# Kernel tuning notes

Hardware: AMD Instinct MI355X
Metric: run time of the kernel (lower is better)

The kernel has to match this reference:

```python
import jax, jax.numpy as jnp
import numpy as np

D = 4096
L = 24
H = 8
HD = D // H
Z_TAU = 3.0
SCALE = 1.0 / float(np.sqrt(HD))


def _ln(x, w=None, b=None, eps=1e-5):
    # torch F.layer_norm over last dim; affine optional
    m = jnp.mean(x, axis=-1, keepdims=True)
    v = jnp.var(x, axis=-1, keepdims=True)
    y = (x - m) * jax.lax.rsqrt(v + eps)
    if w is not None:
        y = y * w + b
    return y


def setup_inputs() -> dict:
    key = jax.random.key(0)
    ks = jax.random.split(key, 16)
    T, N = 512, 2048
    s = 0.02  # init scale for weights
    inp = {
        'text_features': jax.random.normal(ks[0], (T, D), jnp.float32),
        'layer_features': jax.random.normal(ks[1], (L, N, D), jnp.float32),
        # DynamicSharingUnit params
        'layer_embed': jax.random.normal(ks[2], (L, D), jnp.float32) * s,
        'Wc_w': jax.random.normal(ks[3], (2 * D, D), jnp.float32) * s,
        'Wc_b': jnp.zeros((D,), jnp.float32),
        'Wz_w': jax.random.normal(ks[4], (4 * D, D), jnp.float32) * s,
        'Wz_b': jnp.full((D,), -2.0, jnp.float32),
        # SpatialGate params (delta MLP + alpha)
        'd1_w': jax.random.normal(ks[5], (D, D), jnp.float32) * s,
        'd1_b': jnp.zeros((D,), jnp.float32),
        'd2_w': jax.random.normal(ks[6], (D, D), jnp.float32) * s,
        'd2_b': jnp.zeros((D,), jnp.float32),
        'alpha': jnp.asarray(0.5, jnp.float32),
        # attention projections
        'Wq_w': jax.random.normal(ks[7], (D, D), jnp.float32) * s,
        'Wq_b': jnp.zeros((D,), jnp.float32),
        'Wk_w': jax.random.normal(ks[8], (D, D), jnp.float32) * s,
        'Wk_b': jnp.zeros((D,), jnp.float32),
        'Wo_w': jax.random.normal(ks[9], (D, D), jnp.float32) * s,
        'Wo_b': jnp.zeros((D,), jnp.float32),
        # layernorm affine params
        'qn_w': jnp.ones((D,), jnp.float32), 'qn_b': jnp.zeros((D,), jnp.float32),
        'kn_w': jnp.ones((D,), jnp.float32), 'kn_b': jnp.zeros((D,), jnp.float32),
        'vn_w': jnp.ones((D,), jnp.float32), 'vn_b': jnp.zeros((D,), jnp.float32),
        'on_w': jnp.ones((D,), jnp.float32), 'on_b': jnp.zeros((D,), jnp.float32),
    }
    return inp


def reference(text_features, layer_features, layer_embed, Wc_w, Wc_b, Wz_w, Wz_b,
              d1_w, d1_b, d2_w, d2_b, alpha,
              Wq_w, Wq_b, Wk_w, Wk_b, Wo_w, Wo_b,
              qn_w, qn_b, kn_w, kn_b, vn_w, vn_b, on_w, on_b):
    T = text_features.shape[0]
    dt = text_features.dtype

    text_global = _ln(jnp.mean(text_features, axis=0))  # [D]
    y = jnp.mean(layer_features, axis=1)                # [L, D] per-layer means

    # sequential 24-step DynamicSharingUnit recurrence
    def step(c_prev, xs):
        y_l, e_l = xs
        c_tilde = jnp.tanh(jnp.concatenate([y_l, e_l], axis=-1) @ Wc_w + Wc_b)
        z_logit = jnp.concatenate([y_l, c_prev, e_l, text_global], axis=-1) @ Wz_w + Wz_b
        z = jax.nn.sigmoid(z_logit / Z_TAU)
        c_l = c_prev + z * (c_tilde - c_prev)
        return c_l, c_l

    c0 = jnp.zeros((D,), dt)
    _, contexts = jax.lax.scan(step, c0, (y, layer_embed))  # [L, D]

    c_23 = contexts[-2]            # context after layer index 22
    pre_23 = layer_features[-2]    # [N, D]

    # SpatialGate: x + tanh(alpha) * tanh(MLP(LN(x + c)))
    h = _ln(pre_23 + c_23[None, :])
    delta = jnp.tanh(jax.nn.gelu(h @ d1_w + d1_b, approximate=False) @ d2_w + d2_b)
    refreshed = pre_23 + jnp.tanh(alpha) * delta  # [N, D]

    Q = _ln(text_features @ Wq_w + Wq_b, qn_w, qn_b)  # [T, D]
    K = _ln(refreshed @ Wk_w + Wk_b, kn_w, kn_b)      # [N, D]
    V = _ln(refreshed, vn_w, vn_b)                    # [N, D]

    q = Q.reshape(T, H, HD)
    k = K.reshape(-1, H, HD)
    v = V.reshape(-1, H, HD)
    scores = jnp.einsum('thd,nhd->htn', q, k) * SCALE  # [H, T, N]
    w = jax.nn.softmax(scores, axis=-1)
    attn = jnp.einsum('htn,nhd->thd', w, v).reshape(T, D)

    return _ln(attn @ Wo_w + Wo_b, on_w, on_b)  # [T, D]
```

## Files before the change

kernel.cpp:

```cpp
#include <hip/hip_runtime.h>
#include <hip/hip_bf16.h>

constexpr int D_  = 4096;
constexpr int L_  = 24;
constexpr int T_  = 512;
constexpr int N_  = 2048;
constexpr int H_  = 8;
constexpr int HD_ = 512;
constexpr float SCALE_ = 0.04419417382415922f;

typedef __attribute__((ext_vector_type(8))) short short8;
typedef __attribute__((ext_vector_type(4))) float f32x4;

__device__ __forceinline__ unsigned short f2b(float f){
  union{float f; unsigned u;} v; v.f=f;
  return (unsigned short)((v.u + 0x7fffu + ((v.u>>16)&1u))>>16);
}
__device__ __forceinline__ float b2f(unsigned short h){
  union{unsigned u; float f;} v; v.u=((unsigned)h)<<16; return v.f;
}

__device__ __forceinline__ void gload_lds16(const unsigned short* g, unsigned short* l){
  __builtin_amdgcn_global_load_lds((const __attribute__((address_space(1))) unsigned int*)g,
                                   (__attribute__((address_space(3))) unsigned int*)l, 16, 0, 0);
}

struct TP5 { const float* in[5]; unsigned short* out[5]; };

__global__ void prepass_all(TP5 a, const float* __restrict__ wzc_f,
                            unsigned short* __restrict__ wzcb,
                            const float* __restrict__ text,
                            unsigned short* __restrict__ txb){
  const int z = blockIdx.z, t = threadIdx.x;
  if(z < 5){
    __shared__ float tile[64][65];
    const float* in = a.in[z];
    unsigned short* out = a.out[z];
    const int k0 = blockIdx.x*64, n0 = blockIdx.y*64;
    const int rr = t>>4, cc = (t&15)*4;
#pragma unroll
    for(int i=0;i<4;++i){
      const int row = i*16 + rr;
      const float4 v = *(const float4*)(in + (size_t)(k0+row)*D_ + n0 + cc);
      tile[row][cc]=v.x; tile[row][cc+1]=v.y; tile[row][cc+2]=v.z; tile[row][cc+3]=v.w;
    }
    __syncthreads();
#pragma unroll
    for(int i=0;i<4;++i){
      const int row = i*16 + rr;
      unsigned short o4[4] __attribute__((aligned(8)));
      o4[0]=f2b(tile[cc  ][row]);
      o4[1]=f2b(tile[cc+1][row]);
      o4[2]=f2b(tile[cc+2][row]);
      o4[3]=f2b(tile[cc+3][row]);
      *(unsigned long long*)&out[(size_t)(n0+row)*D_ + k0 + cc] = *(const unsigned long long*)o4;
    }
  } else {
    const int bb = blockIdx.y*64 + blockIdx.x;
    const float* in; unsigned short* out; size_t base;
    if(z < 7){ in = wzc_f; out = wzcb; base = ((size_t)(z-5)*4096 + bb)*2048 + (size_t)t*8; }
    else { if(bb >= 1024) return; in = text; out = txb; base = (size_t)bb*2048 + (size_t)t*8; }
    const float4 x0 = *(const float4*)(in + base);
    const float4 x1 = *(const float4*)(in + base + 4);
    unsigned short o[8] __attribute__((aligned(16)));
    o[0]=f2b(x0.x);o[1]=f2b(x0.y);o[2]=f2b(x0.z);o[3]=f2b(x0.w);
    o[4]=f2b(x1.x);o[5]=f2b(x1.y);o[6]=f2b(x1.z);o[7]=f2b(x1.w);
    *(uint4*)(out + base) = *(const uint4*)o;
  }
}

__global__ void transpose_head_b(const unsigned short* __restrict__ in,
                                 unsigned short* __restrict__ out){
  __shared__ unsigned short tile[64][65];
  const int t = threadIdx.x;
  const int h = blockIdx.z;
  const int d0 = blockIdx.x*64, n0 = blockIdx.y*64;
  const int tr = t>>6, tc = t&63;
#pragma unroll
  for(int i=0;i<16;++i) tile[i*4+tr][tc] = in[(size_t)(n0+i*4+tr)*D_ + h*HD_ + d0+tc];
  __syncthreads();
#pragma unroll
  for(int i=0;i<16;++i) out[((size_t)h*HD_ + d0+i*4+tr)*N_ + n0+tc] = tile[tc][i*4+tr];
}

__global__ void colsum_all(const float* __restrict__ layers, const float* __restrict__ text,
                           float* __restrict__ part){
  const int d4 = (blockIdx.x*256 + threadIdx.x)*4;
  const int s = blockIdx.y, z = blockIdx.z;
  const float* p; int rows;
  if(z < 23){ p = layers + (size_t)z*N_*D_ + (size_t)s*(N_/8)*D_ + d4; rows = N_/8; }
  else      { p = text + (size_t)s*(T_/8)*D_ + d4; rows = T_/8; }
  float4 a = {0.f,0.f,0.f,0.f};
  for(int r=0;r<rows;++r){
    const float4 v = *(const float4*)(p + (size_t)r*D_);
    a.x += v.x; a.y += v.y; a.z += v.z; a.w += v.w;
  }
  *(float4*)&part[((size_t)z*8 + s)*D_ + d4] = a;
}

__global__ void reduce_y_gm(const float* __restrict__ part, float* __restrict__ y,
                            float* __restrict__ tg){
  __shared__ float sm[256];
  const int b = blockIdx.x, t = threadIdx.x;
  if(b < 368){
    const int i = b*256 + t, l = i>>12, j = i & (D_-1);
    float a = 0.f;
#pragma unroll
    for(int s=0;s<8;++s) a += part[((size_t)l*8 + s)*D_ + j];
    y[i] = a * (1.f/N_);
    return;
  }
  float v[16]; float sum = 0.f;
#pragma unroll
  for(int c=0;c<16;++c){
    const int j = c*256 + t;
    float a = 0.f;
#pragma unroll
    for(int s=0;s<8;++s) a += part[((size_t)184 + s)*D_ + j];
    v[c] = a * (1.f/T_); sum += v[c];
  }
  sm[t]=sum; __syncthreads();
  for(int o=128;o>0;o>>=1){ if(t<o) sm[t]+=sm[t+o]; __syncthreads(); }
  const float mean = sm[0]*(1.f/D_); __syncthreads();
  float q=0.f;
#pragma unroll
  for(int c=0;c<16;++c){ const float dd=v[c]-mean; q+=dd*dd; }
  sm[t]=q; __syncthreads();
  for(int o=128;o>0;o>>=1){ if(t<o) sm[t]+=sm[t+o]; __syncthreads(); }
  const float rstd = rsqrtf(sm[0]*(1.f/D_) + 1e-5f);
#pragma unroll
  for(int c=0;c<16;++c) tg[c*256+t] = (v[c]-mean)*rstd;
}

__global__ void smallm_all(const float* __restrict__ Wc, const float* __restrict__ Wz,
                           const float* __restrict__ y, const float* __restrict__ e,
                           const float* __restrict__ tg,
                           float* __restrict__ part0, float* __restrict__ part1){
  const int j = (blockIdx.x*256 + threadIdx.x)*2;
  const int sIdx = blockIdx.y;
  const bool w1 = (sIdx >= 16);
  const int s = w1 ? sIdx-16 : sIdx;
  const float* W = w1 ? Wz : Wc;
  const int k0 = s * 512;
  float a0[L_], a1[L_];
#pragma unroll
  for(int l=0;l<L_;++l){ a0[l]=0.f; a1[l]=0.f; }
  __shared__ float xs[L_][64];
  for(int kc=0; kc<512; kc+=64){
    __syncthreads();
    for(int i=threadIdx.x; i<L_*64; i+=256){
      const int l=i>>6, kk=i&63, k=k0+kc+kk;
      float xv;
      if(!w1) xv = (k<D_)? y[(size_t)l*D_+k] : e[(size_t)l*D_ + (k-D_)];
      else    xv = (k<D_)? y[(size_t)l*D_+k]
                : ((k<2*D_)? e[(size_t)l*D_ + (k-D_)] : tg[k-2*D_]);
      xs[l][kk]=xv;
    }
    __syncthreads();
    for(int kk=0;kk<64;++kk){
      const int k=k0+kc+kk;
      const int wrow = w1 ? ((k<D_)? k : k+D_) : k;
      const float2 wv = *(const float2*)&W[(size_t)wrow*D_ + j];
#pragma unroll
      for(int l=0;l<L_;++l){ a0[l] += xs[l][kk]*wv.x; a1[l] += xs[l][kk]*wv.y; }
    }
  }
  float* out = w1 ? part1 : part0;
  const int S = w1 ? 24 : 16;
  for(int l=0;l<L_;++l){
    float2 o; o.x=a0[l]; o.y=a1[l];
    *(float2*)&out[((size_t)l*S + s)*D_ + j] = o;
  }
}

__global__ void reduce_ct_aall(const float* __restrict__ part0, const float* __restrict__ part1,
                               const float* __restrict__ Wcb, const float* __restrict__ Wzb,
                               float* __restrict__ ct, float* __restrict__ aall){
  int b = blockIdx.x;
  const int t = threadIdx.x;
  if(b < 368){
    const int i = b*256+t, l = i>>12, j = i & (D_-1);
    float a = 0.f;
#pragma unroll
    for(int s=0;s<16;++s) a += part0[((size_t)l*16 + s)*D_ + j];
    ct[i] = tanhf(a + Wcb[j]);
  } else {
    b -= 368;
    const int i = b*256+t, l = i>>12, j = i & (D_-1);
    float a = 0.f;
#pragma unroll
    for(int s=0;s<24;++s) a += part1[((size_t)l*24 + s)*D_ + j];
    aall[i] = a + Wzb[j];
  }
}

__device__ __forceinline__ void rec_matvec(const unsigned short* __restrict__ Wzc,
                                           const float* cs, float* red, float* __restrict__ zcur,
                                           int cg, int ks, int t){
  const int k0 = ks*128;
  float acc[8];
#pragma unroll
  for(int q=0;q<8;++q) acc[q]=0.f;
  const int rg = t>>6, oc = t&63;
  const unsigned short* Wb = Wzc + (size_t)(k0+rg*32)*D_ + cg*512 + oc*8;
#pragma unroll
  for(int rr=0;rr<4;++rr){
#pragma unroll
    for(int r=0;r<8;++r){
      const uint4 wv = *(const uint4*)(Wb + (size_t)(rr*8+r)*D_);
      const float cv = cs[rg*32+rr*8+r];
      acc[0]+=cv*b2f((unsigned short)(wv.x&0xffffu));
      acc[1]+=cv*b2f((unsigned short)(wv.x>>16));
      acc[2]+=cv*b2f((unsigned short)(wv.y&0xffffu));
      acc[3]+=cv*b2f((unsigned short)(wv.y>>16));
      acc[4]+=cv*b2f((unsigned short)(wv.z&0xffffu));
      acc[5]+=cv*b2f((unsigned short)(wv.z>>16));
      acc[6]+=cv*b2f((unsigned short)(wv.w&0xffffu));
      acc[7]+=cv*b2f((unsigned short)(wv.w>>16));
    }
  }
#pragma unroll
  for(int q=0;q<8;++q) red[rg*512 + oc*8 + q] = acc[q];
  __syncthreads();
  float s0=0.f, s1=0.f;
#pragma unroll
  for(int g=0;g<4;++g){ s0 += red[g*512 + t]; s1 += red[g*512 + t + 256]; }
  zcur[(size_t)ks*D_ + cg*512 + t]       = s0;
  zcur[(size_t)ks*D_ + cg*512 + t + 256] = s1;
}

__global__ __launch_bounds__(256,2) void rec_first(
    const unsigned short* __restrict__ Wzc, const float* __restrict__ aall0,
    const float* __restrict__ ct0, float* __restrict__ zcur, float* __restrict__ cnew){
  const int blk = blockIdx.x, cg = blk & 7, ks = blk >> 3, t = threadIdx.x;
  const int k0 = ks*128;
  __shared__ float cs[128];
  __shared__ float red[4*512];
  if(t<128){
    const float zl = aall0[k0+t];
    const float z = 1.f/(1.f+expf(-zl*(1.f/3.f)));
    const float cn = z*ct0[k0+t];
    cs[t]=cn; if(cg==0) cnew[k0+t]=cn;
  }
  __syncthreads();
  rec_matvec(Wzc, cs, red, zcur, cg, ks, t);
}

__global__ __launch_bounds__(256,2) void rec_step(
    const unsigned short* __restrict__ Wzc,
    const float* __restrict__ zprev, float* __restrict__ zcur,
    const float* __restrict__ cprev, float* __restrict__ cnew,
    const float* __restrict__ aallL, const float* __restrict__ ctL){
  const int blk = blockIdx.x, cg = blk & 7, ks = blk >> 3, t = threadIdx.x;
  const int k0 = ks*128;
  __shared__ float cs[128];
  __shared__ float red[4*512];
  {
    const int col = t & 127, hf = t >> 7;
    float s=0.f;
#pragma unroll
    for(int si=0;si<16;++si) s += zprev[(size_t)(hf*16+si)*D_ + k0 + col];
    red[hf*128+col] = s;
    __syncthreads();
    if(t<128){
      const float zl = aallL[k0+t] + red[t] + red[128+t];
      const float z = 1.f/(1.f+expf(-zl*(1.f/3.f)));
      const float cp = cprev[k0+t];
      const float cn = cp + z*(ctL[k0+t]-cp);
      cs[t]=cn;
      if(cg==0) cnew[k0+t]=cn;
    }
  }
  __syncthreads();
  rec_matvec(Wzc, cs, red, zcur, cg, ks, t);
}

__global__ void gate_final(const float* __restrict__ zp, const float* __restrict__ cin,
                           const float* __restrict__ aallL, const float* __restrict__ ctL,
                           float* __restrict__ cout){
  const int j = blockIdx.x*256 + threadIdx.x;
  float zl = aallL[j];
  for(int s=0;s<32;++s) zl += zp[(size_t)s*D_ + j];
  const float z = 1.f/(1.f + expf(-zl*(1.f/3.f)));
  const float cp = cin[j];
  cout[j] = cp + z*(ctL[j] - cp);
}

__device__ __forceinline__ void ln_vals(float* v, const float* w, const float* b,
                                        float* of, unsigned short* ob,
                                        bool aff, bool obf, float* sm, int t){
  float s=0.f;
#pragma unroll
  for(int i=0;i<16;++i) s += v[i];
  sm[t]=s; __syncthreads();
  for(int o=128;o>0;o>>=1){ if(t<o) sm[t]+=sm[t+o]; __syncthreads(); }
  const float mean = sm[0]*(1.f/D_); __syncthreads();
  float q=0.f;
#pragma unroll
  for(int i=0;i<16;++i){ const float dd=v[i]-mean; q+=dd*dd; }
  sm[t]=q; __syncthreads();
  for(int o=128;o>0;o>>=1){ if(t<o) sm[t]+=sm[t+o]; __syncthreads(); }
  const float rstd = rsqrtf(sm[0]*(1.f/D_) + 1e-5f);
#pragma unroll
  for(int i=0;i<16;++i){
    const int d = i*256+t;
    float yv=(v[i]-mean)*rstd;
    if(aff) yv = yv*w[d] + b[d];
    if(obf) ob[d] = f2b(yv);
    else    of[d] = yv;
  }
}

template<bool ADDC, bool AFF, bool OBF>
__global__ void row_ln(const float* __restrict__ x, const float* __restrict__ cvec,
                       const float* __restrict__ w, const float* __restrict__ b,
                       float* __restrict__ of, unsigned short* __restrict__ ob){
  __shared__ float sm[256];
  const int row = blockIdx.x, t = threadIdx.x;
  const float* xr = x + (size_t)row*D_;
  float v[16];
#pragma unroll
  for(int i=0;i<16;++i){
    const int d = i*256 + t;
    float val = xr[d];
    if(ADDC) val += cvec[d];
    v[i]=val;
  }
  ln_vals(v, w, b, of? of + (size_t)row*D_ : nullptr,
          ob? ob + (size_t)row*D_ : nullptr, AFF, OBF, sm, t);
}

__global__ void ln3(const float* __restrict__ qpre, const float* __restrict__ refr,
                    const float* __restrict__ kpre, const float* __restrict__ qpb,
                    const float* __restrict__ qnw, const float* __restrict__ qnb,
                    const float* __restrict__ vnw, const float* __restrict__ vnb,
                    const float* __restrict__ knw, const float* __restrict__ knb,
                    unsigned short* __restrict__ qb, unsigned short* __restrict__ vb,
                    unsigned short* __restrict__ kb){
  __shared__ float sm[256];
  const int which = blockIdx.y, row = blockIdx.x, t = threadIdx.x;
  float v[16];
  if(which==0){
    if(row>=T_) return;
    const float* x0 = qpre + (size_t)row*D_;
#pragma unroll
    for(int i=0;i<16;++i){
      const int d = i*256+t;
      v[i] = x0[d] + x0[(size_t)T_*D_ + d] + x0[(size_t)2*T_*D_ + d]
           + x0[(size_t)3*T_*D_ + d] + qpb[d];
    }
    ln_vals(v, qnw, qnb, nullptr, qb + (size_t)row*D_, true, true, sm, t);
  } else {
    const float* x = (which==1)? refr : kpre;
    const float* w = (which==1)? vnw : knw;
    const float* b = (which==1)? vnb : knb;
    unsigned short* o = (which==1)? vb : kb;
    const float* xr = x + (size_t)row*D_;
#pragma unroll
    for(int i=0;i<16;++i) v[i] = xr[i*256+t];
    ln_vals(v, w, b, nullptr, o + (size_t)row*D_, true, true, sm, t);
  }
}

__global__ void row_ln_out(const float* __restrict__ opre, const float* __restrict__ opb,
                           const float* __restrict__ w, const float* __restrict__ b,
                           float* __restrict__ out){
  __shared__ float sm[256];
  const int row = blockIdx.x, t = threadIdx.x;
  const float* x0 = opre + (size_t)row*D_;
  float v[16];
#pragma unroll
  for(int i=0;i<16;++i){
    const int d = i*256+t;
    v[i] = x0[d] + x0[(size_t)T_*D_ + d] + x0[(size_t)2*T_*D_ + d]
         + x0[(size_t)3*T_*D_ + d] + opb[d];
  }
  ln_vals(v, w, b, out + (size_t)row*D_, nullptr, true, false, sm, t);
}

__global__ void softmax_rows(unsigned short* __restrict__ wb){
  __shared__ float sm[256];
  const size_t base = (size_t)blockIdx.x * N_;
  const int t = threadIdx.x;
  float v[8];
  float mx = -3.4e38f;
#pragma unroll
  for(int i=0;i<8;++i){ v[i]=b2f(wb[base + i*256 + t]); mx=fmaxf(mx,v[i]); }
  sm[t]=mx; __syncthreads();
  for(int o=128;o>0;o>>=1){ if(t<o) sm[t]=fmaxf(sm[t],sm[t+o]); __syncthreads(); }
  mx=sm[0]; __syncthreads();
  float s=0.f;
#pragma unroll
  for(int i=0;i<8;++i){ v[i]=expf(v[i]-mx); s+=v[i]; }
  sm[t]=s; __syncthreads();
  for(int o=128;o>0;o>>=1){ if(t<o) sm[t]+=sm[t+o]; __syncthreads(); }
  const float inv = 1.f/sm[0];
#pragma unroll
  for(int i=0;i<8;++i) wb[base + i*256 + t] = f2b(v[i]*inv);
}

enum { EPI_F32_BIAS=0, EPI_BF16_GELU=1, EPI_SPATIAL=2, EPI_BF16_SCALE=3, EPI_BF16=4, EPI_F32_RAW=5 };

constexpr int GBK=32;

template<int EPI, int WM>
__global__ __launch_bounds__(256,2) void gemm_bt(
  const unsigned short* __restrict__ A, const unsigned short* __restrict__ BT,
  const float* __restrict__ bias,
  float* __restrict__ Cf, unsigned short* __restrict__ Cb,
  int M, int Ncols, int K, int lda, int ldb, int ldc,
  long long aZ, long long bZ, long long cZ,
  const float* __restrict__ pre, const float* __restrict__ alphap, float scale)
{
  constexpr int BMt = WM*64;
  constexpr int NF  = WM*2;
  __shared__ unsigned short As[BMt*GBK];
  __shared__ unsigned short Bs[128*GBK];
  const int t = threadIdx.x;
  const int lane = t&63, wid = t>>6;
  const int m0 = blockIdx.x*BMt, n0 = blockIdx.y*128;
  A  += (size_t)blockIdx.z*aZ;
  BT += (size_t)blockIdx.z*bZ;
  const size_t coff = (size_t)blockIdx.z*cZ;

  const int srow = wid*16 + (lane>>2);
  const int scol = (lane&3)*8;
  const unsigned short* ag = A  + (size_t)(m0+srow)*lda + scol;
  const unsigned short* bg = BT + (size_t)(n0+srow)*ldb + scol;
  unsigned short* asl = &As[wid*512];
  unsigned short* bsl = &Bs[wid*512];

  f32x4 acc[4][NF];
#pragma unroll
  for(int i=0;i<4;++i)
#pragma unroll
    for(int j=0;j<NF;++j) acc[i][j]=(f32x4){0.f,0.f,0.f,0.f};

  const int wm = (WM==2)? (wid>>1)*64 : 0;
  const int wn = (WM==2)? (wid&1)*64 : wid*32;
  const int lrow=lane&15, lk=(lane>>4)*8;

  for(int k0=0;k0<K;k0+=GBK){
    __syncthreads();
    gload_lds16(ag + k0, asl);
    if(WM==2) gload_lds16(ag + k0 + (size_t)64*lda, asl + 2048);
    gload_lds16(bg + k0, bsl);
    gload_lds16(bg + k0 + (size_t)64*ldb, bsl + 2048);
    __syncthreads();
    short8 af[4], bfr[NF];
#pragma unroll
    for(int i=0;i<4;++i)  af[i]  = *(const short8*)&As[(wm+i*16+lrow)*GBK + lk];
#pragma unroll
    for(int j=0;j<NF;++j) bfr[j] = *(const short8*)&Bs[(wn+j*16+lrow)*GBK + lk];
#pragma unroll
    for(int i=0;i<4;++i)
#pragma unroll
      for(int j=0;j<NF;++j)
        acc[i][j] = __builtin_amdgcn_mfma_f32_16x16x32_bf16(af[i], bfr[j], acc[i][j], 0,0,0);
  }

#pragma unroll
  for(int i=0;i<4;++i)
#pragma unroll
    for(int j=0;j<NF;++j){
      const int col = n0 + wn + j*16 + lrow;
      const int rb  = m0 + wm + i*16 + (lane>>4)*4;
#pragma unroll
      for(int r=0;r<4;++r){
        const int row = rb + r;
        const float v = acc[i][j][r];
        const size_t idx = coff + (size_t)row*ldc + col;
        if(EPI==EPI_F32_BIAS){ Cf[idx] = v + bias[col]; }
        else { Cb[idx]=f2b(v); }
      }
    }
}

constexpr int P_SLOT_A = 128*64;
constexpr int P_SLOT_B = 256*64;
constexpr int P_SLOT_E = P_SLOT_A + P_SLOT_B;

#define MF16(a,b,c) __builtin_amdgcn_mfma_f32_16x16x32_bf16(a,b,c,0,0,0)

template<int EPI, bool SWZ>
__global__ __launch_bounds__(512,2) void gemm8p(
    const unsigned short* __restrict__ A, const unsigned short* __restrict__ BT,
    const float* __restrict__ bias,
    float* __restrict__ Cf, unsigned short* __restrict__ Cb,
    int K, int lda, int ldb, int ldc,
    long long aZ, long long bZ, long long cZ,
    const float* __restrict__ pre, const float* __restrict__ alphap, float scale)
{
  __shared__ unsigned short lds[3*P_SLOT_E];
  const int tid = threadIdx.x;
  const int lane = tid & 63, wid = tid >> 6;
  int mi, ni, zi;
  if(SWZ){
    const int b = blockIdx.x;
    const int swz = (b & 7)*32 + (b >> 3);
    mi = swz >> 4; ni = swz & 15; zi = 0;
  } else { mi = blockIdx.x; ni = blockIdx.y; zi = blockIdx.z; }
  const int m0 = mi*128, n0 = ni*256;
  A  += (size_t)zi*aZ;
  BT += (size_t)zi*bZ;
  const size_t coff = (size_t)zi*cZ;

  const int wm = (wid >> 2)*64, wn = (wid & 3)*64;
  const int lr = lane & 15, lhi = lane >> 4;

  auto stage = [&](int slot, int kt){
    const int k0 = kt*64;
    unsigned short* sA = lds + slot*P_SLOT_E;
    unsigned short* sB = sA + P_SLOT_A;
#pragma unroll
    for(int q=0;q<2;++q){
      const int o = q*8192 + tid*16;
      const int r = o >> 7;
      const int cb = (o & 127) ^ ((r & 7) << 4);
      gload_lds16(A + (size_t)(m0+r)*lda + k0 + (cb>>1), sA + q*4096 + wid*512);
    }
#pragma unroll
    for(int q=0;q<4;++q){
      const int o = q*8192 + tid*16;
      const int r = o >> 7;
      const int cb = (o & 127) ^ ((r & 7) << 4);
      gload_lds16(BT + (size_t)(n0+r)*ldb + k0 + (cb>>1), sB + q*4096 + wid*512);
    }
  };

  auto ldA = [&](const unsigned short* sA, int i, int ks)->short8{
    const int ra = wm + i*16 + lr;
    const int cb = (ks*64 + lhi*16) ^ ((ra & 7) << 4);
    return *(const short8*)((const char*)sA + ra*128 + cb);
  };
  auto ldB = [&](const unsigned short* sB, int j, int ks)->short8{
    const int rb = wn + j*16 + lr;
    const int cb = (ks*64 + lhi*16) ^ ((rb & 7) << 4);
    return *(const short8*)((const char*)sB + rb*128 + cb);
  };

  f32x4 acc[4][4];
#pragma unroll
  for(int i=0;i<4;++i)
#pragma unroll
    for(int j=0;j<4;++j) acc[i][j]=(f32x4){0.f,0.f,0.f,0.f};

  auto tile_compute = [&](const unsigned short* sA, const unsigned short* sB){
#pragma unroll
    for(int ks=0; ks<2; ++ks){
      short8 a0=ldA(sA,0,ks), a1=ldA(sA,1,ks), a2=ldA(sA,2,ks), a3=ldA(sA,3,ks);
      short8 b0=ldB(sB,0,ks), b1=ldB(sB,1,ks);
      __builtin_amdgcn_s_setprio(1);
      acc[0][0]=MF16(a0,b0,acc[0][0]); acc[1][0]=MF16(a1,b0,acc[1][0]);
      acc[2][0]=MF16(a2,b0,acc[2][0]); acc[3][0]=MF16(a3,b0,acc[3][0]);
      acc[0][1]=MF16(a0,b1,acc[0][1]); acc[1][1]=MF16(a1,b1,acc[1][1]);
      acc[2][1]=MF16(a2,b1,acc[2][1]); acc[3][1]=MF16(a3,b1,acc[3][1]);
      __builtin_amdgcn_s_setprio(0);
      __builtin_amdgcn_s_barrier();
      short8 b2=ldB(sB,2,ks), b3=ldB(sB,3,ks);
      __builtin_amdgcn_s_setprio(1);
      acc[0][2]=MF16(a0,b2,acc[0][2]); acc[1][2]=MF16(a1,b2,acc[1][2]);
      acc[2][2]=MF16(a2,b2,acc[2][2]); acc[3][2]=MF16(a3,b2,acc[3][2]);
      acc[0][3]=MF16(a0,b3,acc[0][3]); acc[1][3]=MF16(a1,b3,acc[1][3]);
      acc[2][3]=MF16(a2,b3,acc[2][3]); acc[3][3]=MF16(a3,b3,acc[3][3]);
      __builtin_amdgcn_s_setprio(0);
      if(ks==0) __builtin_amdgcn_s_barrier();
    }
  };

  const int nt = K >> 6;
  stage(0, 0);
  stage(1, 1);
  int cur = 0;
  for(int t=0; t<nt-1; ++t){
    asm volatile("s_waitcnt vmcnt(6)" ::: "memory");
    __builtin_amdgcn_s_barrier();
    int s2 = cur+2; if(s2>=3) s2-=3;
    if(t+2 < nt) stage(s2, t+2);
    const unsigned short* sA = lds + cur*P_SLOT_E;
    tile_compute(sA, sA + P_SLOT_A);
    ++cur; if(cur==3) cur=0;
  }
  asm volatile("s_waitcnt vmcnt(0)" ::: "memory");
  __builtin_amdgcn_s_barrier();
  {
    const unsigned short* sA = lds + cur*P_SLOT_E;
    tile_compute(sA, sA + P_SLOT_A);
  }

  float ta=0.f;
  if(EPI==EPI_SPATIAL) ta = tanhf(alphap[0]);
#pragma unroll
  for(int i=0;i<4;++i)
#pragma unroll
    for(int j=0;j<4;++j){
      const int col = n0 + wn + j*16 + lr;
      const int rb  = m0 + wm + i*16 + lhi*4;
#pragma unroll
      for(int r=0;r<4;++r){
        const int row = rb + r;
        const float v = acc[i][j][r];
        const size_t idx = coff + (size_t)row*ldc + col;
        if(EPI==EPI_F32_BIAS){ Cf[idx] = v + bias[col]; }
        else if(EPI==EPI_F32_RAW){ Cf[idx] = v; }
        else if(EPI==EPI_BF16_GELU){
          const float x = v + bias[col];
          Cb[idx] = f2b(0.5f*x*(1.f+erff(x*0.70710678118f)));
        }
        else if(EPI==EPI_SPATIAL){
          const float x = tanhf(v + bias[col]);
          const float o = pre[idx] + ta*x;
          Cf[idx]=o; Cb[idx]=f2b(o);
        }
        else if(EPI==EPI_BF16_SCALE){ Cb[idx]=f2b(v*scale); }
      }
    }
}

constexpr size_t OFF_TG   = 0;
constexpr size_t OFF_C    = OFF_TG + (size_t)D_*4;
constexpr size_t OFF_Y    = OFF_C  + (size_t)D_*4;
constexpr size_t OFF_CT   = OFF_Y  + (size_t)L_*D_*4;
constexpr size_t OFF_AA   = OFF_CT + (size_t)L_*D_*4;
constexpr size_t OFF_ZP0  = OFF_AA + (size_t)L_*D_*4;
constexpr size_t OFF_ZP1  = OFF_ZP0 + (size_t)32*D_*4;
constexpr size_t OFF_PART = OFF_ZP1 + (size_t)32*D_*4;
constexpr size_t OFF_QPRE = OFF_PART + (size_t)24*L_*D_*4;
constexpr size_t OFF_REFR = OFF_QPRE + (size_t)4*T_*D_*4;
constexpr size_t OFF_HB   = OFF_REFR + (size_t)N_*D_*4;
constexpr size_t OFF_G1   = OFF_HB + (size_t)N_*D_*2;
constexpr size_t OFF_KPRE = OFF_HB;
constexpr size_t OFF_QB   = OFF_G1 + (size_t)N_*D_*2;
constexpr size_t OFF_KB   = OFF_QB + (size_t)T_*D_*2;
constexpr size_t OFF_VB   = OFF_KB + (size_t)N_*D_*2;
constexpr size_t OFF_VT   = OFF_VB + (size_t)N_*D_*2;
constexpr size_t OFF_WB   = OFF_VT + (size_t)H_*HD_*N_*2;
constexpr size_t OFF_ATTN = OFF_WB + (size_t)H_*T_*N_*2;
constexpr size_t OFF_W1T  = OFF_ATTN + (size_t)T_*D_*2;
constexpr size_t OFF_W2T  = OFF_W1T + (size_t)D_*D_*2;
constexpr size_t OFF_WKT  = OFF_W2T + (size_t)D_*D_*2;
constexpr size_t OFF_WQT  = OFF_WKT + (size_t)D_*D_*2;
constexpr size_t OFF_WOT  = OFF_WQT + (size_t)D_*D_*2;
constexpr size_t OFF_WZCB = OFF_WOT + (size_t)D_*D_*2;
constexpr size_t OFF_TXB  = OFF_WZCB + (size_t)D_*D_*2;
constexpr size_t OFF_REFB = OFF_TXB + (size_t)T_*D_*2;
constexpr size_t OFF_CA   = OFF_REFB + (size_t)N_*D_*2;
constexpr size_t OFF_CB   = OFF_CA + (size_t)D_*4;

extern "C" void kernel_launch(void* const* d_in, const int* in_sizes, int n_in,
                              void* d_out, int out_size, void* d_ws, size_t ws_size,
                              hipStream_t stream){
  (void)in_sizes; (void)n_in; (void)out_size; (void)ws_size;
  const float* text  = (const float*)d_in[0];
  const float* layers= (const float*)d_in[1];
  const float* le    = (const float*)d_in[2];
  const float* Wc    = (const float*)d_in[3];
  const float* Wcb   = (const float*)d_in[4];
  const float* Wz    = (const float*)d_in[5];
  const float* Wzb   = (const float*)d_in[6];
  const float* d1w   = (const float*)d_in[7];
  const float* d1b   = (const float*)d_in[8];
  const float* d2w   = (const float*)d_in[9];
  const float* d2b   = (const float*)d_in[10];
  const float* alpha = (const float*)d_in[11];
  const float* Wqw=(const float*)d_in[12]; const float* Wqb=(const float*)d_in[13];
  const float* Wkw=(const float*)d_in[14]; const float* Wkb=(const float*)d_in[15];
  const float* Wow=(const float*)d_in[16]; const float* Wob=(const float*)d_in[17];
  const float* qnw=(const float*)d_in[18]; const float* qnb=(const float*)d_in[19];
  const float* knw=(const float*)d_in[20]; const float* knb=(const float*)d_in[21];
  const float* vnw=(const float*)d_in[22]; const float* vnb=(const float*)d_in[23];
  const float* onw=(const float*)d_in[24]; const float* onb=(const float*)d_in[25];
  float* out = (float*)d_out;

  char* w = (char*)d_ws;
  float* tg    = (float*)(w + OFF_TG);
  float* cvec  = (float*)(w + OFF_C);
  float* y     = (float*)(w + OFF_Y);
  float* ct    = (float*)(w + OFF_CT);
  float* aall  = (float*)(w + OFF_AA);
  float* zp0   = (float*)(w + OFF_ZP0);
  float* zp1   = (float*)(w + OFF_ZP1);
  float* part  = (float*)(w + OFF_PART);
  float* part1 = part + (size_t)384*D_;
  float* qpre  = (float*)(w + OFF_QPRE);
  float* opre  = qpre;
  float* refr  = (float*)(w + OFF_REFR);
  float* kpre  = (float*)(w + OFF_KPRE);
  float* cA    = (float*)(w + OFF_CA);
  float* cB    = (float*)(w + OFF_CB);
  unsigned short* hb    = (unsigned short*)(w + OFF_HB);
  unsigned short* g1    = (unsigned short*)(w + OFF_G1);
  unsigned short* qb    = (unsigned short*)(w + OFF_QB);
  unsigned short* kb    = (unsigned short*)(w + OFF_KB);
  unsigned short* vb    = (unsigned short*)(w + OFF_VB);
  unsigned short* vt    = (unsigned short*)(w + OFF_VT);
  unsigned short* wb    = (unsigned short*)(w + OFF_WB);
  unsigned short* attnb = (unsigned short*)(w + OFF_ATTN);
  unsigned short* d1t   = (unsigned short*)(w + OFF_W1T);
  unsigned short* d2t   = (unsigned short*)(w + OFF_W2T);
  unsigned short* wkt   = (unsigned short*)(w + OFF_WKT);
  unsigned short* wqt   = (unsigned short*)(w + OFF_WQT);
  unsigned short* wot   = (unsigned short*)(w + OFF_WOT);
  unsigned short* wzcb  = (unsigned short*)(w + OFF_WZCB);
  unsigned short* txb   = (unsigned short*)(w + OFF_TXB);
  unsigned short* refb  = (unsigned short*)(w + OFF_REFB);

  const dim3 b256(256);
  const float* pre23 = layers + (size_t)(L_-2)*N_*D_;

  TP5 tp; tp.in[0]=d1w; tp.in[1]=d2w; tp.in[2]=Wkw; tp.in[3]=Wqw; tp.in[4]=Wow;
  tp.out[0]=d1t; tp.out[1]=d2t; tp.out[2]=wkt; tp.out[3]=wqt; tp.out[4]=wot;
  prepass_all<<<dim3(64,64,8),b256,0,stream>>>(tp, Wz + (size_t)D_*D_, wzcb, text, txb);

  colsum_all<<<dim3(4,8,24),b256,0,stream>>>(layers, text, part);
  reduce_y_gm<<<dim3(369),b256,0,stream>>>(part, y, tg);
  smallm_all<<<dim3(8,40),b256,0,stream>>>(Wc, Wz, y, le, tg, part, part1);
  reduce_ct_aall<<<dim3(736),b256,0,stream>>>(part, part1, Wcb, Wzb, ct, aall);

  rec_first<<<dim3(256),b256,0,stream>>>(wzcb, aall, ct, zp0, cA);
  for(int i=1;i<L_-2;++i){
    float* zprev = (i&1)? zp0 : zp1;
    float* zcur  = (i&1)? zp1 : zp0;
    float* cprev = (i&1)? cA  : cB;
    float* cnew  = (i&1)? cB  : cA;
    rec_step<<<dim3(256),b256,0,stream>>>(wzcb, zprev, zcur, cprev, cnew,
        aall + (size_t)i*D_, ct + (size_t)i*D_);
  }
  gate_final<<<dim3(16),b256,0,stream>>>(zp1, cB,
      aall + (size_t)(L_-2)*D_, ct + (size_t)(L_-2)*D_, cvec);

  row_ln<true,false,true><<<dim3(N_),b256,0,stream>>>(pre23, cvec, nullptr,nullptr, nullptr, hb);
  gemm8p<EPI_BF16_GELU,true><<<dim3(256),dim3(512),0,stream>>>(
      hb, d1t, d1b, nullptr, g1, D_, D_, D_, D_, 0,0,0, nullptr,nullptr,0.f);
  gemm8p<EPI_SPATIAL,true><<<dim3(256),dim3(512),0,stream>>>(
      g1, d2t, d2b, refr, refb, D_, D_, D_, D_, 0,0,0, pre23, alpha, 0.f);

  gemm8p<EPI_F32_RAW,false><<<dim3(4,16,4),dim3(512),0,stream>>>(
      txb, wqt, nullptr, qpre, nullptr, 1024, D_, D_, D_,
      1024, 1024, (long long)T_*D_, nullptr,nullptr,0.f);
  gemm8p<EPI_F32_BIAS,true><<<dim3(256),dim3(512),0,stream>>>(
      refb, wkt, Wkb, kpre, nullptr, D_, D_, D_, D_, 0,0,0, nullptr,nullptr,0.f);

  ln3<<<dim3(N_,3),b256,0,stream>>>(qpre, refr, kpre, Wqb,
      qnw,qnb, vnw,vnb, knw,knb, qb, vb, kb);
  transpose_head_b<<<dim3(8,32,8),b256,0,stream>>>(vb, vt);

  gemm8p<EPI_BF16_SCALE,false><<<dim3(4,8,8),dim3(512),0,stream>>>(
      qb, kb, nullptr, nullptr, wb, HD_, D_, D_, N_,
      (long long)HD_, (long long)HD_, (long long)T_*N_, nullptr,nullptr, SCALE_);
  softmax_rows<<<dim3(H_*T_),b256,0,stream>>>(wb);
  gemm_bt<EPI_BF16,1><<<dim3(8,4,8),b256,0,stream>>>(
      wb, vt, nullptr, nullptr, attnb, T_, HD_, N_, N_, N_, D_,
      (long long)T_*N_, (long long)HD_*N_, (long long)HD_, nullptr,nullptr,0.f);

  gemm8p<EPI_F32_RAW,false><<<dim3(4,16,4),dim3(512),0,stream>>>(
      attnb, wot, nullptr, opre, nullptr, 1024, D_, D_, D_,
      1024, 1024, (long long)T_*D_, nullptr,nullptr,0.f);
  row_ln_out<<<dim3(T_),b256,0,stream>>>(opre, Wob, onw, onb, out);
}
```

Baseline: 1.096 ms.

## Overlap weight transpose-conversion with serial recurrence kernels

```diff
diff --git a/kernel.cpp b/kernel.cpp
--- a/kernel.cpp
+++ b/kernel.cpp
@@ -25,47 +25,48 @@
                                    (__attribute__((address_space(3))) unsigned int*)l, 16, 0, 0);
 }
 
+__global__ void cvt_small(const float* __restrict__ wzc_f, unsigned short* __restrict__ wzcb,
+                          const float* __restrict__ text, unsigned short* __restrict__ txb){
+  const int z = blockIdx.z, t = threadIdx.x;
+  const int bb = blockIdx.y*64 + blockIdx.x;
+  const float* in; unsigned short* out; size_t base;
+  if(z < 2){ in = wzc_f; out = wzcb; base = ((size_t)z*4096 + bb)*2048 + (size_t)t*8; }
+  else { if(bb >= 1024) return; in = text; out = txb; base = (size_t)bb*2048 + (size_t)t*8; }
+  const float4 x0 = *(const float4*)(in + base);
+  const float4 x1 = *(const float4*)(in + base + 4);
+  unsigned short o[8] __attribute__((aligned(16)));
+  o[0]=f2b(x0.x);o[1]=f2b(x0.y);o[2]=f2b(x0.z);o[3]=f2b(x0.w);
+  o[4]=f2b(x1.x);o[5]=f2b(x1.y);o[6]=f2b(x1.z);o[7]=f2b(x1.w);
+  *(uint4*)(out + base) = *(const uint4*)o;
+}
+
 struct TP5 { const float* in[5]; unsigned short* out[5]; };
-
-__global__ void prepass_all(TP5 a, const float* __restrict__ wzc_f,
-                            unsigned short* __restrict__ wzcb,
-                            const float* __restrict__ text,
-                            unsigned short* __restrict__ txb){
-  const int z = blockIdx.z, t = threadIdx.x;
-  if(z < 5){
-    __shared__ float tile[64][65];
-    const float* in = a.in[z];
-    unsigned short* out = a.out[z];
-    const int k0 = blockIdx.x*64, n0 = blockIdx.y*64;
-    const int rr = t>>4, cc = (t&15)*4;
-#pragma unroll
-    for(int i=0;i<4;++i){
-      const int row = i*16 + rr;
-      const float4 v = *(const float4*)(in + (size_t)(k0+row)*D_ + n0 + cc);
-      tile[row][cc]=v.x; tile[row][cc+1]=v.y; tile[row][cc+2]=v.z; tile[row][cc+3]=v.w;
-    }
-    __syncthreads();
-#pragma unroll
-    for(int i=0;i<4;++i){
-      const int row = i*16 + rr;
-      unsigned short o4[4] __attribute__((aligned(8)));
-      o4[0]=f2b(tile[cc  ][row]);
-      o4[1]=f2b(tile[cc+1][row]);
-      o4[2]=f2b(tile[cc+2][row]);
-      o4[3]=f2b(tile[cc+3][row]);
-      *(unsigned long long*)&out[(size_t)(n0+row)*D_ + k0 + cc] = *(const unsigned long long*)o4;
-    }
-  } else {
-    const int bb = blockIdx.y*64 + blockIdx.x;
-    const float* in; unsigned short* out; size_t base;
-    if(z < 7){ in = wzc_f; out = wzcb; base = ((size_t)(z-5)*4096 + bb)*2048 + (size_t)t*8; }
-    else { if(bb >= 1024) return; in = text; out = txb; base = (size_t)bb*2048 + (size_t)t*8; }
-    const float4 x0 = *(const float4*)(in + base);
-    const float4 x1 = *(const float4*)(in + base + 4);
-    unsigned short o[8] __attribute__((aligned(16)));
-    o[0]=f2b(x0.x);o[1]=f2b(x0.y);o[2]=f2b(x0.z);o[3]=f2b(x0.w);
-    o[4]=f2b(x1.x);o[5]=f2b(x1.y);o[6]=f2b(x1.z);o[7]=f2b(x1.w);
-    *(uint4*)(out + base) = *(const uint4*)o;
+constexpr int TP_TILES = 5*4096;
+constexpr int TP_CHUNK = 931;
+
+__device__ __forceinline__ void do_transpose_tile(const TP5& a, int idx, float* shm, int t){
+  const int z = idx >> 12, rem = idx & 4095;
+  const int k0 = (rem >> 6)*64, n0 = (rem & 63)*64;
+  const float* in = a.in[z];
+  unsigned short* out = a.out[z];
+  float (*tile)[65] = (float(*)[65])shm;
+  const int rr = t>>4, cc = (t&15)*4;
+#pragma unroll
+  for(int i=0;i<4;++i){
+    const int row = i*16 + rr;
+    const float4 v = *(const float4*)(in + (size_t)(k0+row)*D_ + n0 + cc);
+    tile[row][cc]=v.x; tile[row][cc+1]=v.y; tile[row][cc+2]=v.z; tile[row][cc+3]=v.w;
+  }
+  __syncthreads();
+#pragma unroll
+  for(int i=0;i<4;++i){
+    const int row = i*16 + rr;
+    unsigned short o4[4] __attribute__((aligned(8)));
+    o4[0]=f2b(tile[cc  ][row]);
+    o4[1]=f2b(tile[cc+1][row]);
+    o4[2]=f2b(tile[cc+2][row]);
+    o4[3]=f2b(tile[cc+3][row]);
+    *(unsigned long long*)&out[(size_t)(n0+row)*D_ + k0 + cc] = *(const unsigned long long*)o4;
   }
 }
 
@@ -231,11 +232,18 @@
 
 __global__ __launch_bounds__(256,2) void rec_first(
     const unsigned short* __restrict__ Wzc, const float* __restrict__ aall0,
-    const float* __restrict__ ct0, float* __restrict__ zcur, float* __restrict__ cnew){
-  const int blk = blockIdx.x, cg = blk & 7, ks = blk >> 3, t = threadIdx.x;
+    const float* __restrict__ ct0, float* __restrict__ zcur, float* __restrict__ cnew,
+    TP5 tp, int tbase){
+  __shared__ float shm[64*65];
+  const int blk = blockIdx.x, t = threadIdx.x;
+  if(blk >= 256){
+    const int idx = tbase + blk - 256;
+    if(idx < TP_TILES) do_transpose_tile(tp, idx, shm, t);
+    return;
+  }
+  const int cg = blk & 7, ks = blk >> 3;
   const int k0 = ks*128;
-  __shared__ float cs[128];
-  __shared__ float red[4*512];
+  float* cs = shm; float* red = shm + 128;
   if(t<128){
     const float zl = aall0[k0+t];
     const float z = 1.f/(1.f+expf(-zl*(1.f/3.f)));
@@ -250,11 +258,18 @@
     const unsigned short* __restrict__ Wzc,
     const float* __restrict__ zprev, float* __restrict__ zcur,
     const float* __restrict__ cprev, float* __restrict__ cnew,
-    const float* __restrict__ aallL, const float* __restrict__ ctL){
-  const int blk = blockIdx.x, cg = blk & 7, ks = blk >> 3, t = threadIdx.x;
+    const float* __restrict__ aallL, const float* __restrict__ ctL,
+    TP5 tp, int tbase){
+  __shared__ float shm[64*65];
+  const int blk = blockIdx.x, t = threadIdx.x;
+  if(blk >= 256){
+    const int idx = tbase + blk - 256;
+    if(idx < TP_TILES) do_transpose_tile(tp, idx, shm, t);
+    return;
+  }
+  const int cg = blk & 7, ks = blk >> 3;
   const int k0 = ks*128;
-  __shared__ float cs[128];
-  __shared__ float red[4*512];
+  float* cs = shm; float* red = shm + 128;
   {
     const int col = t & 127, hf = t >> 7;
     float s=0.f;
@@ -710,21 +725,22 @@
 
   TP5 tp; tp.in[0]=d1w; tp.in[1]=d2w; tp.in[2]=Wkw; tp.in[3]=Wqw; tp.in[4]=Wow;
   tp.out[0]=d1t; tp.out[1]=d2t; tp.out[2]=wkt; tp.out[3]=wqt; tp.out[4]=wot;
-  prepass_all<<<dim3(64,64,8),b256,0,stream>>>(tp, Wz + (size_t)D_*D_, wzcb, text, txb);
+
+  cvt_small<<<dim3(64,64,3),b256,0,stream>>>(Wz + (size_t)D_*D_, wzcb, text, txb);
 
   colsum_all<<<dim3(4,8,24),b256,0,stream>>>(layers, text, part);
   reduce_y_gm<<<dim3(369),b256,0,stream>>>(part, y, tg);
   smallm_all<<<dim3(8,40),b256,0,stream>>>(Wc, Wz, y, le, tg, part, part1);
   reduce_ct_aall<<<dim3(736),b256,0,stream>>>(part, part1, Wcb, Wzb, ct, aall);
 
-  rec_first<<<dim3(256),b256,0,stream>>>(wzcb, aall, ct, zp0, cA);
+  rec_first<<<dim3(256+TP_CHUNK),b256,0,stream>>>(wzcb, aall, ct, zp0, cA, tp, 0);
   for(int i=1;i<L_-2;++i){
     float* zprev = (i&1)? zp0 : zp1;
     float* zcur  = (i&1)? zp1 : zp0;
     float* cprev = (i&1)? cA  : cB;
     float* cnew  = (i&1)? cB  : cA;
-    rec_step<<<dim3(256),b256,0,stream>>>(wzcb, zprev, zcur, cprev, cnew,
-        aall + (size_t)i*D_, ct + (size_t)i*D_);
+    rec_step<<<dim3(256+TP_CHUNK),b256,0,stream>>>(wzcb, zprev, zcur, cprev, cnew,
+        aall + (size_t)i*D_, ct + (size_t)i*D_, tp, i*TP_CHUNK);
   }
   gate_final<<<dim3(16),b256,0,stream>>>(zp1, cB,
       aall + (size_t)(L_-2)*D_, ct + (size_t)(L_-2)*D_, cvec);
```

Measured after the change: 1.067 ms. 2.6% less time.
